# Kernel optimization log

Measured on AMD Instinct MI355X. Metric: run time of the kernel, lower is better.

## Reference

```python
import jax, jax.numpy as jnp
import numpy as np

D = 512  # common_dim

def _ln(x, g, b):
    m = jnp.mean(x, -1, keepdims=True)
    v = jnp.var(x, -1, keepdims=True)
    return g * (x - m) * jax.lax.rsqrt(v + 1e-5) + b

def _gelu(x):
    return jax.nn.gelu(x, approximate=False)  # torch nn.GELU default (erf)

def _mha(q, kv, Wi, bi, Wo, bo):
    # seq_len == 1: softmax over a single key is exactly 1 regardless of q/k,
    # so MultiheadAttention reduces to out_proj(v_proj(kv)); identical math,
    # and q/k projections receive exactly zero gradient either way.
    vp = kv @ Wi[:, 2 * D:] + bi[2 * D:]
    return vp @ Wo + bo

def setup_inputs() -> dict:
    key = jax.random.key(0)
    ks = iter(jax.random.split(key, 64))
    B, HID = 8192, 1024
    Fv, Fi, Ft = 10, 6, 15
    def rn(shape, s=0.02):
        return jax.random.normal(next(ks), shape, jnp.float32) * s
    return dict(
        verb_hidden=rn((B, HID), 1.0), verb_logits=rn((B, Fv), 1.0),
        inst_hidden=rn((B, HID), 1.0), inst_logits=rn((B, Fi), 1.0),
        target_hidden=rn((B, HID), 1.0), target_logits=rn((B, Ft), 1.0),
        # hidden_projection per task (order: verb, instrument, target)
        hp_W=rn((3, HID, D)), hp_b=jnp.zeros((3, D)), hp_g=jnp.ones((3, D)), hp_be=jnp.zeros((3, D)),
        # logit_projection per task (different in-dims)
        lp_W_verb=rn((Fv, D // 2)), lp_b_verb=jnp.zeros((D // 2,)),
        lp_W_inst=rn((Fi, D // 2)), lp_b_inst=jnp.zeros((D // 2,)),
        lp_W_target=rn((Ft, D // 2)), lp_b_target=jnp.zeros((D // 2,)),
        lp_g=jnp.ones((3, D // 2)), lp_be=jnp.zeros((3, D // 2)),
        # 4 MHA modules: [self, verb_inst, verb_target, inst_target]
        mha_in_W=rn((4, D, 3 * D)), mha_in_b=jnp.zeros((4, 3 * D)),
        mha_out_W=rn((4, D, D)), mha_out_b=jnp.zeros((4, D)),
        n1_g=jnp.ones((3, D)), n1_be=jnp.zeros((3, D)),
        n2_g=jnp.ones((3, D)), n2_be=jnp.zeros((3, D)),
        gate_W=rn((3, 2 * D, D)), gate_b=jnp.zeros((3, D)),
        fus_W1=rn((3 * D + 3 * (D // 2), D)), fus_b1=jnp.zeros((D,)),
        fus_g1=jnp.ones((D,)), fus_ge1=jnp.zeros((D,)),
        fus_W2=rn((D, D)), fus_b2=jnp.zeros((D,)),
        fus_g2=jnp.ones((D,)), fus_ge2=jnp.zeros((D,)),
    )

def reference(verb_hidden, verb_logits, inst_hidden, inst_logits, target_hidden, target_logits,
              hp_W, hp_b, hp_g, hp_be,
              lp_W_verb, lp_b_verb, lp_W_inst, lp_b_inst, lp_W_target, lp_b_target, lp_g, lp_be,
              mha_in_W, mha_in_b, mha_out_W, mha_out_b,
              n1_g, n1_be, n2_g, n2_be, gate_W, gate_b,
              fus_W1, fus_b1, fus_g1, fus_ge1, fus_W2, fus_b2, fus_g2, fus_ge2):
    # dropout is inference-mode identity
    def hproj(x, i):
        return _gelu(_ln(x @ hp_W[i] + hp_b[i], hp_g[i], hp_be[i]))
    def lproj(x, W, b, i):
        return _gelu(_ln(jax.nn.sigmoid(x) @ W + b, lp_g[i], lp_be[i]))

    verb_h, inst_h, target_h = hproj(verb_hidden, 0), hproj(inst_hidden, 1), hproj(target_hidden, 2)
    verb_l = lproj(verb_logits, lp_W_verb, lp_b_verb, 0)
    inst_l = lproj(inst_logits, lp_W_inst, lp_b_inst, 1)
    target_l = lproj(target_logits, lp_W_target, lp_b_target, 2)

    sa = lambda x: _mha(x, x, mha_in_W[0], mha_in_b[0], mha_out_W[0], mha_out_b[0])
    verb_e = _ln(verb_h + sa(verb_h), n1_g[0], n1_be[0])
    inst_e = _ln(inst_h + sa(inst_h), n1_g[1], n1_be[1])
    target_e = _ln(target_h + sa(target_h), n1_g[2], n1_be[2])

    ca = lambda i, q, kv: _mha(q, kv, mha_in_W[i], mha_in_b[i], mha_out_W[i], mha_out_b[i])
    v2i, i2v = ca(1, verb_e, inst_e), ca(1, inst_e, verb_e)
    v2t, t2v = ca(2, verb_e, target_e), ca(2, target_e, verb_e)
    i2t, t2i = ca(3, inst_e, target_e), ca(3, target_e, inst_e)

    def fuse(x, a, b, i):
        m = (a + b) * 0.5
        gate = jax.nn.sigmoid(jnp.concatenate([x, m], axis=1) @ gate_W[i] + gate_b[i])
        return _ln(x + gate * m, n2_g[i], n2_be[i])

    verb_f = fuse(verb_e, v2i, v2t, 0)
    inst_f = fuse(inst_e, i2v, i2t, 1)
    target_f = fuse(target_e, t2v, t2i, 2)

    comb = jnp.concatenate([verb_f, inst_f, target_f, verb_l, inst_l, target_l], axis=1)  # [B, 2304]
    h = _gelu(_ln(comb @ fus_W1 + fus_b1, fus_g1, fus_ge1))
    return _ln(h @ fus_W2 + fus_b2, fus_g2, fus_ge2)
```

## Files before the change

kernel.cpp:

```cpp
#include <hip/hip_runtime.h>
#include <math.h>

typedef unsigned short ushort_t;
using short8  = __attribute__((ext_vector_type(8))) short;
using floatx4 = __attribute__((ext_vector_type(4))) float;

__device__ __forceinline__ ushort_t f2bf(float f) {
  unsigned u = __builtin_bit_cast(unsigned, f);
  u = (u + 0x7fffu + ((u >> 16) & 1u)) >> 16;
  return (ushort_t)u;
}
__device__ __forceinline__ float bf2f(ushort_t u) {
  unsigned v = ((unsigned)u) << 16;
  return __builtin_bit_cast(float, v);
}

__device__ __forceinline__ void load_lds16(const ushort_t* g, ushort_t* l) {
  __builtin_amdgcn_global_load_lds(
      (const __attribute__((address_space(1))) unsigned int*)g,
      (__attribute__((address_space(3))) unsigned int*)l, 16, 0, 0);
}

struct Seg { const ushort_t* A; const ushort_t* W; int lda, ldw, K; };
struct GemmZ {
  ushort_t* Cb;
  ushort_t* CbT;
  const float* bias;
  float scale; int nseg; int mmax;
  Seg seg[6];
};
struct GemmArgs { GemmZ z[9]; };

template <int BM>
__global__ __launch_bounds__(256) void gemm_bt(GemmArgs ga) {
  const GemmZ& gz = ga.z[blockIdx.z];
  if ((int)blockIdx.x >= gz.mmax) return;
  __shared__ ushort_t As[BM * 32];
  __shared__ ushort_t Bs[128 * 32];
  const int tid = threadIdx.x;
  const int wid = tid >> 6, lane = tid & 63, quad = lane >> 4, l16 = lane & 15;
  const int bm = blockIdx.x * BM, bn = blockIdx.y * 128;
  constexpr int MI = BM / 32;
  const int wm = (wid & 1) * (BM / 2), wn = (wid >> 1) * 64;
  floatx4 acc[MI][4] = {};
  const int srow = tid >> 2, scol = (tid & 3) * 8;
  ushort_t* aL = As + tid * 8;
  ushort_t* bL = Bs + tid * 8;

  for (int s = 0; s < gz.nseg; s++) {
    const Seg sg = gz.seg[s];
    const ushort_t* aG = sg.A + (size_t)(bm + srow) * sg.lda + scol;
    const ushort_t* bG = sg.W + (size_t)(bn + srow) * sg.ldw + scol;
    const size_t astep = (size_t)64 * sg.lda;
    const size_t bstep = (size_t)64 * sg.ldw;
    for (int k0 = 0; k0 < sg.K; k0 += 32) {
      __syncthreads();
      load_lds16(aG + k0, aL);
      if (BM == 128) load_lds16(aG + k0 + astep, aL + 2048);
      load_lds16(bG + k0, bL);
      load_lds16(bG + k0 + bstep, bL + 2048);
      __syncthreads();
      short8 af[MI], bf[4];
#pragma unroll
      for (int i = 0; i < MI; i++)
        af[i] = *(const short8*)&As[(wm + 16 * i + l16) * 32 + quad * 8];
#pragma unroll
      for (int j = 0; j < 4; j++)
        bf[j] = *(const short8*)&Bs[(wn + 16 * j + l16) * 32 + quad * 8];
#pragma unroll
      for (int i = 0; i < MI; i++)
#pragma unroll
        for (int j = 0; j < 4; j++)
          acc[i][j] = __builtin_amdgcn_mfma_f32_16x16x32_bf16(af[i], bf[j], acc[i][j], 0, 0, 0);
    }
  }

#pragma unroll
  for (int i = 0; i < MI; i++) {
#pragma unroll
    for (int j = 0; j < 4; j++) {
      const int colg = bn + wn + 16 * j + l16;
      const float bb = gz.bias ? gz.bias[colg] : 0.f;
#pragma unroll
      for (int r = 0; r < 4; r++) {
        const int rowg = bm + wm + 16 * i + quad * 4 + r;
        const float v = (acc[i][j][r] + bb) * gz.scale;
        const ushort_t bo = f2bf(v);
        if (gz.Cb)  gz.Cb[(size_t)rowg * 512 + colg] = bo;
        if (gz.CbT) gz.CbT[(size_t)colg * 512 + rowg] = bo;
      }
    }
  }
}

__global__ __launch_bounds__(256) void row_ln(
    const ushort_t* __restrict__ P, const ushort_t* __restrict__ R,
    const ushort_t* __restrict__ cross,
    const float* __restrict__ gamma, const float* __restrict__ beta, int gstride,
    ushort_t* __restrict__ outb, float* __restrict__ outf, int mode, int gelu)
{
  const size_t S2 = (size_t)8192 * 512;
  const int wid = threadIdx.x >> 6, lane = threadIdx.x & 63;
  const int row = blockIdx.x * 4 + wid;
  const int t = row >> 13;
  const float* g  = gamma + t * gstride;
  const float* be = beta + t * gstride;
  const ushort_t* p = P + (size_t)row * 512;
  const ushort_t* ar = nullptr;
  if (mode == 2) ar = cross + (size_t)(2 * t) * S2 + (size_t)(row & 8191) * 512;
  float v[8], s = 0.f, ss = 0.f;
#pragma unroll
  for (int j = 0; j < 8; j++) {
    const int c = lane + j * 64;
    float x = bf2f(p[c]);
    if (mode == 2) {
      const float sg = 1.f / (1.f + expf(-x));
      x = bf2f(R[(size_t)row * 512 + c]) + sg * (bf2f(ar[c]) + bf2f(ar[S2 + c]));
    } else if (mode == 1) {
      x += bf2f(R[(size_t)row * 512 + c]);
    }
    v[j] = x; s += x; ss += x * x;
  }
#pragma unroll
  for (int off = 32; off > 0; off >>= 1) {
    s  += __shfl_xor(s,  off, 64);
    ss += __shfl_xor(ss, off, 64);
  }
  const float mean = s * (1.f / 512.f);
  const float var  = ss * (1.f / 512.f) - mean * mean;
  const float rstd = rsqrtf(var + 1e-5f);
#pragma unroll
  for (int j = 0; j < 8; j++) {
    const int c = lane + j * 64;
    float y = g[c] * ((v[j] - mean) * rstd) + be[c];
    if (gelu) y = 0.5f * y * (1.f + erff(y * 0.70710678118f));
    if (outb) outb[(size_t)row * 512 + c] = f2bf(y);
    else      outf[(size_t)row * 512 + c] = y;
  }
}

__global__ __launch_bounds__(256) void lproj3(
    const float* __restrict__ vl, const float* __restrict__ il, const float* __restrict__ tl,
    const float* __restrict__ Wv, const float* __restrict__ bv,
    const float* __restrict__ Wi, const float* __restrict__ bi,
    const float* __restrict__ Wt, const float* __restrict__ bt,
    const float* __restrict__ lp_g, const float* __restrict__ lp_be,
    ushort_t* __restrict__ out)
{
  const int set = blockIdx.y;
  const float* logits = set == 0 ? vl : set == 1 ? il : tl;
  const int F = set == 0 ? 10 : set == 1 ? 6 : 15;
  const float* W    = set == 0 ? Wv : set == 1 ? Wi : Wt;
  const float* bias = set == 0 ? bv : set == 1 ? bi : bt;
  const float* gamma = lp_g + set * 256;
  const float* beta  = lp_be + set * 256;
  ushort_t* o = out + (size_t)set * 8192 * 256;
  const int wid = threadIdx.x >> 6, lane = threadIdx.x & 63;
  const int row = blockIdx.x * 4 + wid;
  float sg[16];
  for (int f = 0; f < F; f++)
    sg[f] = 1.f / (1.f + expf(-logits[(size_t)row * F + f]));
  float v[4], s = 0.f, ss = 0.f;
#pragma unroll
  for (int j = 0; j < 4; j++) {
    const int c = lane + j * 64;
    float a = bias[c];
    for (int f = 0; f < F; f++) a += sg[f] * W[f * 256 + c];
    v[j] = a; s += a; ss += a * a;
  }
#pragma unroll
  for (int off = 32; off > 0; off >>= 1) {
    s  += __shfl_xor(s,  off, 64);
    ss += __shfl_xor(ss, off, 64);
  }
  const float mean = s * (1.f / 256.f);
  const float var  = ss * (1.f / 256.f) - mean * mean;
  const float rstd = rsqrtf(var + 1e-5f);
#pragma unroll
  for (int j = 0; j < 4; j++) {
    const int c = lane + j * 64;
    float y = gamma[c] * ((v[j] - mean) * rstd) + beta[c];
    y = 0.5f * y * (1.f + erff(y * 0.70710678118f));
    o[(size_t)row * 256 + c] = f2bf(y);
  }
}

struct PrepArgs {
  const float *vh, *ih, *th;
  const float *mha_in_W, *mha_out_W, *mha_in_b, *mha_out_b;
  const float *hp_W, *gate_W, *fus_W1, *fus_W2;
  ushort_t *xbf, *Wvbf, *hpWt, *gateWt, *fusW1t, *fusW2t, *WoT;
  float *cb;
};

__global__ __launch_bounds__(256) void prep(PrepArgs pa) {
  __shared__ float tsh[32][33];
  const int b = blockIdx.x, tid = threadIdx.x;
  if (b < 24576) {
    const int mat = b >> 13, blk = b & 8191;
    const float* src = mat == 0 ? pa.vh : mat == 1 ? pa.ih : pa.th;
    const size_t i = (size_t)blk * 256 + tid;
    const float4 f = ((const float4*)src)[i];
    ushort4 o; o.x = f2bf(f.x); o.y = f2bf(f.y); o.z = f2bf(f.z); o.w = f2bf(f.w);
    ((ushort4*)(pa.xbf + (size_t)mat * 8192 * 1024))[i] = o;
    return;
  }
  if (b < 28672) {
    const int u = b - 24576, z = u >> 10, blk = u & 1023;
    const int idx = blk * 256 + tid, r = idx >> 9, c = idx & 511;
    pa.Wvbf[(size_t)z * 262144 + idx] =
        f2bf(pa.mha_in_W[(size_t)z * 786432 + (size_t)r * 1536 + 1024 + c]);
    return;
  }
  if (b >= 34176) {
    const int u2 = b - 34176, z = u2 >> 1, part = u2 & 1;
    const int n = part * 256 + tid;
    const float* bv = pa.mha_in_b + z * 1536 + 1024;
    const float* Wo = pa.mha_out_W + (size_t)z * 262144;
    float a = pa.mha_out_b[z * 512 + n];
    for (int k = 0; k < 512; k++) a += bv[k] * Wo[(size_t)k * 512 + n];
    pa.cb[z * 512 + n] = a;
    return;
  }
  const float* tin; ushort_t* tout; int K, N, u; size_t izs, ozs;
  if (b < 30208)      { u = b - 28672; tin = pa.hp_W;      tout = pa.hpWt;   K = 1024; N = 512; izs = 524288; ozs = 524288; }
  else if (b < 31744) { u = b - 30208; tin = pa.gate_W;    tout = pa.gateWt; K = 1024; N = 512; izs = 524288; ozs = 524288; }
  else if (b < 32896) { u = b - 31744; tin = pa.fus_W1;    tout = pa.fusW1t; K = 2304; N = 512; izs = 0;      ozs = 0; }
  else if (b < 33152) { u = b - 32896; tin = pa.fus_W2;    tout = pa.fusW2t; K = 512;  N = 512; izs = 0;      ozs = 0; }
  else                { u = b - 33152; tin = pa.mha_out_W; tout = pa.WoT;    K = 512;  N = 512; izs = 262144; ozs = 262144; }
  const int nbx = N / 32, perz = nbx * (K / 32);
  const int z = u / perz, rem = u % perz, bx = rem % nbx, by = rem / nbx;
  tin += (size_t)z * izs; tout += (size_t)z * ozs;
  const int n0 = bx * 32, k0 = by * 32;
  const int tx = tid & 31, ty = tid >> 5;
#pragma unroll
  for (int r = 0; r < 32; r += 8)
    tsh[ty + r][tx] = tin[(size_t)(k0 + ty + r) * N + n0 + tx];
  __syncthreads();
#pragma unroll
  for (int r = 0; r < 32; r += 8)
    tout[(size_t)(n0 + ty + r) * K + k0 + tx] = f2bf(tsh[tx][ty + r]);
}

__global__ __launch_bounds__(256) void bias2_k(
    const float* __restrict__ cb, const float* __restrict__ gate_W,
    const float* __restrict__ gate_b, float* __restrict__ out)
{
  const int t = blockIdx.z;
  const int m1[3] = {1, 1, 2}, m2[3] = {2, 3, 3};
  const float* c1 = cb + m1[t] * 512;
  const float* c2 = cb + m2[t] * 512;
  const float* W = gate_W + (size_t)t * 524288 + (size_t)512 * 512;
  const int n = blockIdx.x * 256 + threadIdx.x;
  float a = gate_b[t * 512 + n];
  for (int k = 0; k < 512; k++) a += 0.5f * (c1[k] + c2[k]) * W[(size_t)k * 512 + n];
  out[t * 512 + n] = a;
}

extern "C" void kernel_launch(void* const* d_in, const int* in_sizes, int n_in,
                              void* d_out, int out_size, void* d_ws, size_t ws_size,
                              hipStream_t stream)
{
  const float* verb_hidden   = (const float*)d_in[0];
  const float* verb_logits   = (const float*)d_in[1];
  const float* inst_hidden   = (const float*)d_in[2];
  const float* inst_logits   = (const float*)d_in[3];
  const float* target_hidden = (const float*)d_in[4];
  const float* target_logits = (const float*)d_in[5];
  const float* hp_W  = (const float*)d_in[6];
  const float* hp_b  = (const float*)d_in[7];
  const float* hp_g  = (const float*)d_in[8];
  const float* hp_be = (const float*)d_in[9];
  const float* lp_W_verb   = (const float*)d_in[10];
  const float* lp_b_verb   = (const float*)d_in[11];
  const float* lp_W_inst   = (const float*)d_in[12];
  const float* lp_b_inst   = (const float*)d_in[13];
  const float* lp_W_target = (const float*)d_in[14];
  const float* lp_b_target = (const float*)d_in[15];
  const float* lp_g  = (const float*)d_in[16];
  const float* lp_be = (const float*)d_in[17];
  const float* mha_in_W  = (const float*)d_in[18];
  const float* mha_in_b  = (const float*)d_in[19];
  const float* mha_out_W = (const float*)d_in[20];
  const float* mha_out_b = (const float*)d_in[21];
  const float* n1_g  = (const float*)d_in[22];
  const float* n1_be = (const float*)d_in[23];
  const float* n2_g  = (const float*)d_in[24];
  const float* n2_be = (const float*)d_in[25];
  const float* gate_W = (const float*)d_in[26];
  const float* gate_b = (const float*)d_in[27];
  const float* fus_W1 = (const float*)d_in[28];
  const float* fus_b1 = (const float*)d_in[29];
  const float* fus_g1 = (const float*)d_in[30];
  const float* fus_ge1= (const float*)d_in[31];
  const float* fus_W2 = (const float*)d_in[32];
  const float* fus_b2 = (const float*)d_in[33];
  const float* fus_g2 = (const float*)d_in[34];
  const float* fus_ge2= (const float*)d_in[35];

  char* w = (char*)d_ws;
  const size_t S2 = (size_t)8192 * 512;
  const size_t MB = 1024 * 1024;
  ushort_t* xbf     = (ushort_t*)(w);
  ushort_t* crossbf = (ushort_t*)(w);
  ushort_t* gbf     = (ushort_t*)(w);
  ushort_t* Pbig    = (ushort_t*)(w + 48 * MB);
  ushort_t* hbf     = (ushort_t*)(w + 72 * MB);
  ushort_t* fbf     = (ushort_t*)(w + 72 * MB);
  ushort_t* ebf     = (ushort_t*)(w + 96 * MB);
  ushort_t* lbf     = (ushort_t*)(w + 120 * MB);
  char* wp = w + 132 * MB;
  ushort_t* hpWt    = (ushort_t*)(wp);
  ushort_t* gateWt  = (ushort_t*)(wp + 3145728);
  ushort_t* fusW1t  = (ushort_t*)(wp + 6291456);
  ushort_t* fusW2t  = (ushort_t*)(wp + 8650752);
  ushort_t* WoT     = (ushort_t*)(wp + 9175040);
  ushort_t* Wvbf    = (ushort_t*)(wp + 11272192);
  ushort_t* CWt     = (ushort_t*)(wp + 13369344);
  ushort_t* CWplain = (ushort_t*)(wp + 15466496);
  ushort_t* Gt      = (ushort_t*)(wp + 17563648);
  float*    cb      = (float*)(wp + 20709376);
  float*    bias2   = (float*)(wp + 20717568);

  dim3 blk(256);
  const int mods[3][2] = {{1, 2}, {1, 3}, {2, 3}};
  const int srcs[3][2] = {{1, 2}, {0, 2}, {0, 1}};

  {
    PrepArgs pa;
    pa.vh = verb_hidden; pa.ih = inst_hidden; pa.th = target_hidden;
    pa.mha_in_W = mha_in_W; pa.mha_out_W = mha_out_W;
    pa.mha_in_b = mha_in_b; pa.mha_out_b = mha_out_b;
    pa.hp_W = hp_W; pa.gate_W = gate_W; pa.fus_W1 = fus_W1; pa.fus_W2 = fus_W2;
    pa.xbf = xbf; pa.Wvbf = Wvbf; pa.hpWt = hpWt; pa.gateWt = gateWt;
    pa.fusW1t = fusW1t; pa.fusW2t = fusW2t; pa.WoT = WoT; pa.cb = cb;
    prep<<<34184, blk, 0, stream>>>(pa);
  }

  {
    GemmArgs ga{};
    for (int z = 0; z < 4; z++) {
      GemmZ& g = ga.z[z];
      g.Cb = CWplain + (size_t)z * 262144; g.CbT = CWt + (size_t)z * 262144;
      g.scale = 1.f; g.nseg = 1; g.mmax = 4;
      g.seg[0] = {Wvbf + (size_t)z * 262144, WoT + (size_t)z * 262144, 512, 512, 512};
    }
    gemm_bt<128><<<dim3(4, 4, 4), blk, 0, stream>>>(ga);
  }

  bias2_k<<<dim3(2, 1, 3), blk, 0, stream>>>(cb, gate_W, gate_b, bias2);

  {
    GemmArgs ga{};
    for (int z = 0; z < 3; z++) {
      GemmZ& g = ga.z[z];
      g.Cb = Pbig + (size_t)z * S2; g.bias = hp_b + z * 512;
      g.scale = 1.f; g.nseg = 1; g.mmax = 64;
      g.seg[0] = {xbf + (size_t)z * 8192 * 1024, hpWt + (size_t)z * 524288, 1024, 1024, 1024};
    }
    for (int idx = 0; idx < 6; idx++) {
      const int t = idx >> 1, u = idx & 1, m = mods[t][u];
      GemmZ& g = ga.z[3 + idx];
      g.Cb = Gt + (size_t)idx * 262144; g.scale = 0.5f; g.nseg = 1; g.mmax = 4;
      g.seg[0] = {gateWt + (size_t)t * 524288 + 512, CWplain + (size_t)m * 262144, 1024, 512, 512};
    }
    gemm_bt<128><<<dim3(64, 4, 9), blk, 0, stream>>>(ga);
  }

  lproj3<<<dim3(2048, 3), blk, 0, stream>>>(verb_logits, inst_logits, target_logits,
      lp_W_verb, lp_b_verb, lp_W_inst, lp_b_inst, lp_W_target, lp_b_target,
      lp_g, lp_be, lbf);

  row_ln<<<6144, blk, 0, stream>>>(Pbig, nullptr, nullptr, hp_g, hp_be, 512,
                                   hbf, nullptr, 0, 1);

  {
    GemmArgs ga{};
    GemmZ& g = ga.z[0];
    g.Cb = Pbig; g.bias = cb; g.scale = 1.f; g.nseg = 1; g.mmax = 192;
    g.seg[0] = {hbf, CWt, 512, 512, 512};
    gemm_bt<128><<<dim3(192, 4, 1), blk, 0, stream>>>(ga);
  }
  row_ln<<<6144, blk, 0, stream>>>(Pbig, hbf, nullptr, n1_g, n1_be, 512,
                                   ebf, nullptr, 1, 0);

  {
    GemmArgs ga{};
    for (int t = 0; t < 3; t++)
      for (int u = 0; u < 2; u++) {
        GemmZ& g = ga.z[2 * t + u];
        g.Cb = crossbf + (size_t)(2 * t + u) * S2;
        g.bias = cb + mods[t][u] * 512; g.scale = 0.5f; g.nseg = 1; g.mmax = 64;
        g.seg[0] = {ebf + (size_t)srcs[t][u] * S2, CWt + (size_t)mods[t][u] * 262144, 512, 512, 512};
      }
    for (int t = 0; t < 3; t++) {
      GemmZ& g = ga.z[6 + t];
      g.Cb = Pbig + (size_t)t * S2; g.bias = bias2 + t * 512;
      g.scale = 1.f; g.nseg = 3; g.mmax = 64;
      g.seg[0] = {ebf + (size_t)t * S2,           gateWt + (size_t)t * 524288, 512, 1024, 512};
      g.seg[1] = {ebf + (size_t)srcs[t][0] * S2,  Gt + (size_t)(2 * t) * 262144,     512, 512, 512};
      g.seg[2] = {ebf + (size_t)srcs[t][1] * S2,  Gt + (size_t)(2 * t + 1) * 262144, 512, 512, 512};
    }
    gemm_bt<128><<<dim3(64, 4, 9), blk, 0, stream>>>(ga);
  }

  row_ln<<<6144, blk, 0, stream>>>(Pbig, ebf, crossbf, n2_g, n2_be, 512,
                                   fbf, nullptr, 2, 0);

  {
    GemmArgs ga{};
    GemmZ& g = ga.z[0];
    g.Cb = Pbig; g.bias = fus_b1; g.scale = 1.f; g.nseg = 6; g.mmax = 128;
    g.seg[0] = {fbf,                          fusW1t,        512, 2304, 512};
    g.seg[1] = {fbf + S2,                     fusW1t + 512,  512, 2304, 512};
    g.seg[2] = {fbf + 2 * S2,                 fusW1t + 1024, 512, 2304, 512};
    g.seg[3] = {lbf,                          fusW1t + 1536, 256, 2304, 256};
    g.seg[4] = {lbf + (size_t)8192 * 256,     fusW1t + 1792, 256, 2304, 256};
    g.seg[5] = {lbf + (size_t)2 * 8192 * 256, fusW1t + 2048, 256, 2304, 256};
    gemm_bt<64><<<dim3(128, 4, 1), blk, 0, stream>>>(ga);
  }
  row_ln<<<2048, blk, 0, stream>>>(Pbig, nullptr, nullptr, fus_g1, fus_ge1, 0,
                                   gbf, nullptr, 0, 1);
  {
    GemmArgs ga{};
    GemmZ& g = ga.z[0];
    g.Cb = Pbig; g.bias = fus_b2; g.scale = 1.f; g.nseg = 1; g.mmax = 128;
    g.seg[0] = {gbf, fusW2t, 512, 512, 512};
    gemm_bt<64><<<dim3(128, 4, 1), blk, 0, stream>>>(ga);
  }
  row_ln<<<2048, blk, 0, stream>>>(Pbig, nullptr, nullptr, fus_g2, fus_ge2, 0,
                                   nullptr, (float*)d_out, 0, 0);
}
```

Measured before the change: 669.8 us.

## Fuse LayerNorm epilogues into full-row GEMM and convert fp32 inputs in-kernel

Replaces the tiled GEMM plus separate row LayerNorm kernels with one GEMM kernel that computes a full 512-wide output row block (32 rows × 512 cols, 512 threads). Residual add, sigmoid gating, LayerNorm and GELU are done in the epilogue through a cross-wave LDS reduction. This removes the bf16 intermediate round trips through global memory and the separate row_ln launches. The hidden-projection GEMM now reads the fp32 inputs directly and converts them to bf16 while staging, so the prep conversion pass is dropped. In exchange, M tiles are smaller (32 rows), each block holds the whole 512×32 B tile, and the fp32 A path uses narrow non-vectorized loads, which could hurt GEMM efficiency.

```diff
diff --git a/kernel.cpp b/kernel.cpp
--- a/kernel.cpp
+++ b/kernel.cpp
@@ -14,129 +14,159 @@
   unsigned v = ((unsigned)u) << 16;
   return __builtin_bit_cast(float, v);
 }
-
 __device__ __forceinline__ void load_lds16(const ushort_t* g, ushort_t* l) {
   __builtin_amdgcn_global_load_lds(
       (const __attribute__((address_space(1))) unsigned int*)g,
       (__attribute__((address_space(3))) unsigned int*)l, 16, 0, 0);
 }
 
-struct Seg { const ushort_t* A; const ushort_t* W; int lda, ldw, K; };
+struct Seg { const void* A; const ushort_t* W; int lda, ldw, K, a_f32; };
 struct GemmZ {
-  ushort_t* Cb;
-  ushort_t* CbT;
+  ushort_t* Cb; ushort_t* CbT; float* Cf;
   const float* bias;
-  float scale; int nseg; int mmax;
+  const ushort_t* R; const ushort_t* crA; const ushort_t* crB;
+  const float* gamma; const float* beta;
+  float scale; int gstride;
+  int nseg, mmax, mode, gelu;
   Seg seg[6];
 };
 struct GemmArgs { GemmZ z[9]; };
 
-template <int BM>
-__global__ __launch_bounds__(256) void gemm_bt(GemmArgs ga) {
+__global__ __launch_bounds__(512) void gemm_fln(GemmArgs ga) {
   const GemmZ& gz = ga.z[blockIdx.z];
   if ((int)blockIdx.x >= gz.mmax) return;
-  __shared__ ushort_t As[BM * 32];
-  __shared__ ushort_t Bs[128 * 32];
+  __shared__ ushort_t Bs[512 * 32];
+  __shared__ ushort_t As[32 * 32];
+  __shared__ float redS[32][8], redSS[32][8];
+  __shared__ float lnM[32], lnR[32];
   const int tid = threadIdx.x;
   const int wid = tid >> 6, lane = tid & 63, quad = lane >> 4, l16 = lane & 15;
-  const int bm = blockIdx.x * BM, bn = blockIdx.y * 128;
-  constexpr int MI = BM / 32;
-  const int wm = (wid & 1) * (BM / 2), wn = (wid >> 1) * 64;
-  floatx4 acc[MI][4] = {};
-  const int srow = tid >> 2, scol = (tid & 3) * 8;
-  ushort_t* aL = As + tid * 8;
-  ushort_t* bL = Bs + tid * 8;
+  const int bm = blockIdx.x * 32;
+  const int wn = wid * 64;
+  floatx4 acc[2][4] = {};
 
   for (int s = 0; s < gz.nseg; s++) {
     const Seg sg = gz.seg[s];
-    const ushort_t* aG = sg.A + (size_t)(bm + srow) * sg.lda + scol;
-    const ushort_t* bG = sg.W + (size_t)(bn + srow) * sg.ldw + scol;
-    const size_t astep = (size_t)64 * sg.lda;
-    const size_t bstep = (size_t)64 * sg.ldw;
     for (int k0 = 0; k0 < sg.K; k0 += 32) {
       __syncthreads();
-      load_lds16(aG + k0, aL);
-      if (BM == 128) load_lds16(aG + k0 + astep, aL + 2048);
-      load_lds16(bG + k0, bL);
-      load_lds16(bG + k0 + bstep, bL + 2048);
+#pragma unroll
+      for (int q = 0; q < 4; q++)
+        load_lds16(sg.W + (size_t)(q * 128 + (tid >> 2)) * sg.ldw + k0 + (tid & 3) * 8,
+                   Bs + q * 4096 + tid * 8);
+      if (sg.a_f32) {
+        const float* Af = (const float*)sg.A;
+        const int ar = tid >> 4, ak = (tid & 15) * 2;
+        const float* src = Af + (size_t)(bm + ar) * sg.lda + k0 + ak;
+        ushort2 h; h.x = f2bf(src[0]); h.y = f2bf(src[1]);
+        *(ushort2*)&As[ar * 32 + ak] = h;
+      } else if (tid < 128) {
+        load_lds16((const ushort_t*)sg.A + (size_t)(bm + (tid >> 2)) * sg.lda + k0 + (tid & 3) * 8,
+                   As + tid * 8);
+      }
       __syncthreads();
-      short8 af[MI], bf[4];
-#pragma unroll
-      for (int i = 0; i < MI; i++)
-        af[i] = *(const short8*)&As[(wm + 16 * i + l16) * 32 + quad * 8];
+      short8 af[2], bf[4];
+#pragma unroll
+      for (int i = 0; i < 2; i++)
+        af[i] = *(const short8*)&As[(16 * i + l16) * 32 + quad * 8];
 #pragma unroll
       for (int j = 0; j < 4; j++)
         bf[j] = *(const short8*)&Bs[(wn + 16 * j + l16) * 32 + quad * 8];
 #pragma unroll
-      for (int i = 0; i < MI; i++)
+      for (int i = 0; i < 2; i++)
 #pragma unroll
         for (int j = 0; j < 4; j++)
           acc[i][j] = __builtin_amdgcn_mfma_f32_16x16x32_bf16(af[i], bf[j], acc[i][j], 0, 0, 0);
     }
   }
 
-#pragma unroll
-  for (int i = 0; i < MI; i++) {
+  if (gz.mode < 0) {
+#pragma unroll
+    for (int i = 0; i < 2; i++)
+#pragma unroll
+      for (int j = 0; j < 4; j++) {
+        const int col = wn + 16 * j + l16;
+        const float bb = gz.bias ? gz.bias[col] : 0.f;
+#pragma unroll
+        for (int r = 0; r < 4; r++) {
+          const int rowg = bm + 16 * i + quad * 4 + r;
+          const ushort_t bo = f2bf((acc[i][j][r] + bb) * gz.scale);
+          if (gz.Cb)  gz.Cb[(size_t)rowg * 512 + col] = bo;
+          if (gz.CbT) gz.CbT[(size_t)col * 512 + rowg] = bo;
+        }
+      }
+    return;
+  }
+
+  const int task = gz.gstride ? (bm >> 13) : 0;
+  const float* gam = gz.gamma + task * gz.gstride;
+  const float* bet = gz.beta  + task * gz.gstride;
+
+  float s_p[2][4] = {}, ss_p[2][4] = {};
+#pragma unroll
+  for (int i = 0; i < 2; i++)
 #pragma unroll
     for (int j = 0; j < 4; j++) {
-      const int colg = bn + wn + 16 * j + l16;
-      const float bb = gz.bias ? gz.bias[colg] : 0.f;
+      const int col = wn + 16 * j + l16;
+      const float bb = gz.bias ? gz.bias[col] : 0.f;
 #pragma unroll
       for (int r = 0; r < 4; r++) {
-        const int rowg = bm + wm + 16 * i + quad * 4 + r;
-        const float v = (acc[i][j][r] + bb) * gz.scale;
-        const ushort_t bo = f2bf(v);
-        if (gz.Cb)  gz.Cb[(size_t)rowg * 512 + colg] = bo;
-        if (gz.CbT) gz.CbT[(size_t)colg * 512 + rowg] = bo;
-      }
-    }
-  }
-}
-
-__global__ __launch_bounds__(256) void row_ln(
-    const ushort_t* __restrict__ P, const ushort_t* __restrict__ R,
-    const ushort_t* __restrict__ cross,
-    const float* __restrict__ gamma, const float* __restrict__ beta, int gstride,
-    ushort_t* __restrict__ outb, float* __restrict__ outf, int mode, int gelu)
-{
-  const size_t S2 = (size_t)8192 * 512;
-  const int wid = threadIdx.x >> 6, lane = threadIdx.x & 63;
-  const int row = blockIdx.x * 4 + wid;
-  const int t = row >> 13;
-  const float* g  = gamma + t * gstride;
-  const float* be = beta + t * gstride;
-  const ushort_t* p = P + (size_t)row * 512;
-  const ushort_t* ar = nullptr;
-  if (mode == 2) ar = cross + (size_t)(2 * t) * S2 + (size_t)(row & 8191) * 512;
-  float v[8], s = 0.f, ss = 0.f;
-#pragma unroll
-  for (int j = 0; j < 8; j++) {
-    const int c = lane + j * 64;
-    float x = bf2f(p[c]);
-    if (mode == 2) {
-      const float sg = 1.f / (1.f + expf(-x));
-      x = bf2f(R[(size_t)row * 512 + c]) + sg * (bf2f(ar[c]) + bf2f(ar[S2 + c]));
-    } else if (mode == 1) {
-      x += bf2f(R[(size_t)row * 512 + c]);
-    }
-    v[j] = x; s += x; ss += x * x;
-  }
-#pragma unroll
-  for (int off = 32; off > 0; off >>= 1) {
-    s  += __shfl_xor(s,  off, 64);
-    ss += __shfl_xor(ss, off, 64);
-  }
-  const float mean = s * (1.f / 512.f);
-  const float var  = ss * (1.f / 512.f) - mean * mean;
-  const float rstd = rsqrtf(var + 1e-5f);
-#pragma unroll
-  for (int j = 0; j < 8; j++) {
-    const int c = lane + j * 64;
-    float y = g[c] * ((v[j] - mean) * rstd) + be[c];
-    if (gelu) y = 0.5f * y * (1.f + erff(y * 0.70710678118f));
-    if (outb) outb[(size_t)row * 512 + c] = f2bf(y);
-    else      outf[(size_t)row * 512 + c] = y;
-  }
+        const int rowg = bm + 16 * i + quad * 4 + r;
+        float x = acc[i][j][r] + bb;
+        if (gz.mode == 1) {
+          x += bf2f(gz.R[(size_t)rowg * 512 + col]);
+        } else if (gz.mode == 2) {
+          const float sg = 1.f / (1.f + expf(-x));
+          x = bf2f(gz.R[(size_t)rowg * 512 + col]) +
+              sg * (bf2f(gz.crA[(size_t)rowg * 512 + col]) +
+                    bf2f(gz.crB[(size_t)rowg * 512 + col]));
+        }
+        acc[i][j][r] = x;
+        s_p[i][r] += x; ss_p[i][r] += x * x;
+      }
+    }
+#pragma unroll
+  for (int m = 1; m <= 8; m <<= 1)
+#pragma unroll
+    for (int i = 0; i < 2; i++)
+#pragma unroll
+      for (int r = 0; r < 4; r++) {
+        s_p[i][r]  += __shfl_xor(s_p[i][r],  m, 64);
+        ss_p[i][r] += __shfl_xor(ss_p[i][r], m, 64);
+      }
+  if (l16 == 0) {
+#pragma unroll
+    for (int i = 0; i < 2; i++)
+#pragma unroll
+      for (int r = 0; r < 4; r++) {
+        redS[16 * i + quad * 4 + r][wid]  = s_p[i][r];
+        redSS[16 * i + quad * 4 + r][wid] = ss_p[i][r];
+      }
+  }
+  __syncthreads();
+  if (tid < 32) {
+    float s = 0.f, ss = 0.f;
+#pragma unroll
+    for (int wv = 0; wv < 8; wv++) { s += redS[tid][wv]; ss += redSS[tid][wv]; }
+    const float mean = s * (1.f / 512.f);
+    const float var  = ss * (1.f / 512.f) - mean * mean;
+    lnM[tid] = mean; lnR[tid] = rsqrtf(var + 1e-5f);
+  }
+  __syncthreads();
+#pragma unroll
+  for (int i = 0; i < 2; i++)
+#pragma unroll
+    for (int j = 0; j < 4; j++) {
+      const int col = wn + 16 * j + l16;
+#pragma unroll
+      for (int r = 0; r < 4; r++) {
+        const int rl = 16 * i + quad * 4 + r;
+        const int rowg = bm + rl;
+        float y = gam[col] * ((acc[i][j][r] - lnM[rl]) * lnR[rl]) + bet[col];
+        if (gz.gelu) y = 0.5f * y * (1.f + erff(y * 0.70710678118f));
+        if (gz.Cf) gz.Cf[(size_t)rowg * 512 + col] = y;
+        else       gz.Cb[(size_t)rowg * 512 + col] = f2bf(y);
+      }
+    }
 }
 
 __global__ __launch_bounds__(256) void lproj3(
@@ -186,34 +216,24 @@
 }
 
 struct PrepArgs {
-  const float *vh, *ih, *th;
   const float *mha_in_W, *mha_out_W, *mha_in_b, *mha_out_b;
   const float *hp_W, *gate_W, *fus_W1, *fus_W2;
-  ushort_t *xbf, *Wvbf, *hpWt, *gateWt, *fusW1t, *fusW2t, *WoT;
+  ushort_t *Wvbf, *hpWt, *gateWt, *fusW1t, *fusW2t, *WoT;
   float *cb;
 };
 
 __global__ __launch_bounds__(256) void prep(PrepArgs pa) {
   __shared__ float tsh[32][33];
   const int b = blockIdx.x, tid = threadIdx.x;
-  if (b < 24576) {
-    const int mat = b >> 13, blk = b & 8191;
-    const float* src = mat == 0 ? pa.vh : mat == 1 ? pa.ih : pa.th;
-    const size_t i = (size_t)blk * 256 + tid;
-    const float4 f = ((const float4*)src)[i];
-    ushort4 o; o.x = f2bf(f.x); o.y = f2bf(f.y); o.z = f2bf(f.z); o.w = f2bf(f.w);
-    ((ushort4*)(pa.xbf + (size_t)mat * 8192 * 1024))[i] = o;
-    return;
-  }
-  if (b < 28672) {
-    const int u = b - 24576, z = u >> 10, blk = u & 1023;
+  if (b < 4096) {
+    const int z = b >> 10, blk = b & 1023;
     const int idx = blk * 256 + tid, r = idx >> 9, c = idx & 511;
     pa.Wvbf[(size_t)z * 262144 + idx] =
         f2bf(pa.mha_in_W[(size_t)z * 786432 + (size_t)r * 1536 + 1024 + c]);
     return;
   }
-  if (b >= 34176) {
-    const int u2 = b - 34176, z = u2 >> 1, part = u2 & 1;
+  if (b >= 9600) {
+    const int u2 = b - 9600, z = u2 >> 1, part = u2 & 1;
     const int n = part * 256 + tid;
     const float* bv = pa.mha_in_b + z * 1536 + 1024;
     const float* Wo = pa.mha_out_W + (size_t)z * 262144;
@@ -223,11 +243,11 @@
     return;
   }
   const float* tin; ushort_t* tout; int K, N, u; size_t izs, ozs;
-  if (b < 30208)      { u = b - 28672; tin = pa.hp_W;      tout = pa.hpWt;   K = 1024; N = 512; izs = 524288; ozs = 524288; }
-  else if (b < 31744) { u = b - 30208; tin = pa.gate_W;    tout = pa.gateWt; K = 1024; N = 512; izs = 524288; ozs = 524288; }
-  else if (b < 32896) { u = b - 31744; tin = pa.fus_W1;    tout = pa.fusW1t; K = 2304; N = 512; izs = 0;      ozs = 0; }
-  else if (b < 33152) { u = b - 32896; tin = pa.fus_W2;    tout = pa.fusW2t; K = 512;  N = 512; izs = 0;      ozs = 0; }
-  else                { u = b - 33152; tin = pa.mha_out_W; tout = pa.WoT;    K = 512;  N = 512; izs = 262144; ozs = 262144; }
+  if (b < 5632)      { u = b - 4096; tin = pa.hp_W;      tout = pa.hpWt;   K = 1024; N = 512; izs = 524288; ozs = 524288; }
+  else if (b < 7168) { u = b - 5632; tin = pa.gate_W;    tout = pa.gateWt; K = 1024; N = 512; izs = 524288; ozs = 524288; }
+  else if (b < 8320) { u = b - 7168; tin = pa.fus_W1;    tout = pa.fusW1t; K = 2304; N = 512; izs = 0;      ozs = 0; }
+  else if (b < 8576) { u = b - 8320; tin = pa.fus_W2;    tout = pa.fusW2t; K = 512;  N = 512; izs = 0;      ozs = 0; }
+  else               { u = b - 8576; tin = pa.mha_out_W; tout = pa.WoT;    K = 512;  N = 512; izs = 262144; ozs = 262144; }
   const int nbx = N / 32, perz = nbx * (K / 32);
   const int z = u / perz, rem = u % perz, bx = rem % nbx, by = rem / nbx;
   tin += (size_t)z * izs; tout += (size_t)z * ozs;
@@ -301,15 +321,13 @@
   char* w = (char*)d_ws;
   const size_t S2 = (size_t)8192 * 512;
   const size_t MB = 1024 * 1024;
-  ushort_t* xbf     = (ushort_t*)(w);
   ushort_t* crossbf = (ushort_t*)(w);
   ushort_t* gbf     = (ushort_t*)(w);
-  ushort_t* Pbig    = (ushort_t*)(w + 48 * MB);
-  ushort_t* hbf     = (ushort_t*)(w + 72 * MB);
-  ushort_t* fbf     = (ushort_t*)(w + 72 * MB);
-  ushort_t* ebf     = (ushort_t*)(w + 96 * MB);
-  ushort_t* lbf     = (ushort_t*)(w + 120 * MB);
-  char* wp = w + 132 * MB;
+  ushort_t* hbf     = (ushort_t*)(w + 48 * MB);
+  ushort_t* fbf     = (ushort_t*)(w + 48 * MB);
+  ushort_t* ebf     = (ushort_t*)(w + 72 * MB);
+  ushort_t* lbf     = (ushort_t*)(w + 96 * MB);
+  char* wp = w + 108 * MB;
   ushort_t* hpWt    = (ushort_t*)(wp);
   ushort_t* gateWt  = (ushort_t*)(wp + 3145728);
   ushort_t* fusW1t  = (ushort_t*)(wp + 6291456);
@@ -322,19 +340,18 @@
   float*    cb      = (float*)(wp + 20709376);
   float*    bias2   = (float*)(wp + 20717568);
 
-  dim3 blk(256);
+  dim3 blk256(256), blk512(512);
   const int mods[3][2] = {{1, 2}, {1, 3}, {2, 3}};
   const int srcs[3][2] = {{1, 2}, {0, 2}, {0, 1}};
 
   {
     PrepArgs pa;
-    pa.vh = verb_hidden; pa.ih = inst_hidden; pa.th = target_hidden;
     pa.mha_in_W = mha_in_W; pa.mha_out_W = mha_out_W;
     pa.mha_in_b = mha_in_b; pa.mha_out_b = mha_out_b;
     pa.hp_W = hp_W; pa.gate_W = gate_W; pa.fus_W1 = fus_W1; pa.fus_W2 = fus_W2;
-    pa.xbf = xbf; pa.Wvbf = Wvbf; pa.hpWt = hpWt; pa.gateWt = gateWt;
+    pa.Wvbf = Wvbf; pa.hpWt = hpWt; pa.gateWt = gateWt;
     pa.fusW1t = fusW1t; pa.fusW2t = fusW2t; pa.WoT = WoT; pa.cb = cb;
-    prep<<<34184, blk, 0, stream>>>(pa);
+    prep<<<9608, blk256, 0, stream>>>(pa);
   }
 
   {
@@ -342,47 +359,46 @@
     for (int z = 0; z < 4; z++) {
       GemmZ& g = ga.z[z];
       g.Cb = CWplain + (size_t)z * 262144; g.CbT = CWt + (size_t)z * 262144;
-      g.scale = 1.f; g.nseg = 1; g.mmax = 4;
-      g.seg[0] = {Wvbf + (size_t)z * 262144, WoT + (size_t)z * 262144, 512, 512, 512};
-    }
-    gemm_bt<128><<<dim3(4, 4, 4), blk, 0, stream>>>(ga);
-  }
-
-  bias2_k<<<dim3(2, 1, 3), blk, 0, stream>>>(cb, gate_W, gate_b, bias2);
-
-  {
-    GemmArgs ga{};
+      g.scale = 1.f; g.nseg = 1; g.mmax = 16; g.mode = -1;
+      g.seg[0] = {Wvbf + (size_t)z * 262144, WoT + (size_t)z * 262144, 512, 512, 512, 0};
+    }
+    gemm_fln<<<dim3(16, 1, 4), blk512, 0, stream>>>(ga);
+  }
+
+  bias2_k<<<dim3(2, 1, 3), blk256, 0, stream>>>(cb, gate_W, gate_b, bias2);
+
+  {
+    GemmArgs ga{};
+    const float* xs[3] = {verb_hidden, inst_hidden, target_hidden};
     for (int z = 0; z < 3; z++) {
       GemmZ& g = ga.z[z];
-      g.Cb = Pbig + (size_t)z * S2; g.bias = hp_b + z * 512;
-      g.scale = 1.f; g.nseg = 1; g.mmax = 64;
-      g.seg[0] = {xbf + (size_t)z * 8192 * 1024, hpWt + (size_t)z * 524288, 1024, 1024, 1024};
+      g.Cb = hbf + (size_t)z * S2; g.bias = hp_b + z * 512;
+      g.gamma = hp_g + z * 512; g.beta = hp_be + z * 512;
+      g.scale = 1.f; g.nseg = 1; g.mmax = 256; g.mode = 0; g.gelu = 1;
+      g.seg[0] = {xs[z], hpWt + (size_t)z * 524288, 1024, 1024, 1024, 1};
     }
     for (int idx = 0; idx < 6; idx++) {
       const int t = idx >> 1, u = idx & 1, m = mods[t][u];
       GemmZ& g = ga.z[3 + idx];
-      g.Cb = Gt + (size_t)idx * 262144; g.scale = 0.5f; g.nseg = 1; g.mmax = 4;
-      g.seg[0] = {gateWt + (size_t)t * 524288 + 512, CWplain + (size_t)m * 262144, 1024, 512, 512};
-    }
-    gemm_bt<128><<<dim3(64, 4, 9), blk, 0, stream>>>(ga);
-  }
-
-  lproj3<<<dim3(2048, 3), blk, 0, stream>>>(verb_logits, inst_logits, target_logits,
+      g.Cb = Gt + (size_t)idx * 262144; g.scale = 0.5f; g.nseg = 1; g.mmax = 16; g.mode = -1;
+      g.seg[0] = {gateWt + (size_t)t * 524288 + 512, CWplain + (size_t)m * 262144, 1024, 512, 512, 0};
+    }
+    gemm_fln<<<dim3(256, 1, 9), blk512, 0, stream>>>(ga);
+  }
+
+  lproj3<<<dim3(2048, 3), blk256, 0, stream>>>(verb_logits, inst_logits, target_logits,
       lp_W_verb, lp_b_verb, lp_W_inst, lp_b_inst, lp_W_target, lp_b_target,
       lp_g, lp_be, lbf);
 
-  row_ln<<<6144, blk, 0, stream>>>(Pbig, nullptr, nullptr, hp_g, hp_be, 512,
-                                   hbf, nullptr, 0, 1);
-
   {
     GemmArgs ga{};
     GemmZ& g = ga.z[0];
-    g.Cb = Pbig; g.bias = cb; g.scale = 1.f; g.nseg = 1; g.mmax = 192;
-    g.seg[0] = {hbf, CWt, 512, 512, 512};
-    gemm_bt<128><<<dim3(192, 4, 1), blk, 0, stream>>>(ga);
-  }
-  row_ln<<<6144, blk, 0, stream>>>(Pbig, hbf, nullptr, n1_g, n1_be, 512,
-                                   ebf, nullptr, 1, 0);
+    g.Cb = ebf; g.bias = cb; g.R = hbf;
+    g.gamma = n1_g; g.beta = n1_be; g.gstride = 512;
+    g.scale = 1.f; g.nseg = 1; g.mmax = 768; g.mode = 1;
+    g.seg[0] = {hbf, CWt, 512, 512, 512, 0};
+    gemm_fln<<<dim3(768, 1, 1), blk512, 0, stream>>>(ga);
+  }
 
   {
     GemmArgs ga{};
@@ -390,44 +406,52 @@
       for (int u = 0; u < 2; u++) {
         GemmZ& g = ga.z[2 * t + u];
         g.Cb = crossbf + (size_t)(2 * t + u) * S2;
-        g.bias = cb + mods[t][u] * 512; g.scale = 0.5f; g.nseg = 1; g.mmax = 64;
-        g.seg[0] = {ebf + (size_t)srcs[t][u] * S2, CWt + (size_t)mods[t][u] * 262144, 512, 512, 512};
-      }
+        g.bias = cb + mods[t][u] * 512; g.scale = 0.5f;
+        g.nseg = 1; g.mmax = 256; g.mode = -1;
+        g.seg[0] = {ebf + (size_t)srcs[t][u] * S2, CWt + (size_t)mods[t][u] * 262144, 512, 512, 512, 0};
+      }
+    gemm_fln<<<dim3(256, 1, 6), blk512, 0, stream>>>(ga);
+  }
+
+  {
+    GemmArgs ga{};
     for (int t = 0; t < 3; t++) {
-      GemmZ& g = ga.z[6 + t];
-      g.Cb = Pbig + (size_t)t * S2; g.bias = bias2 + t * 512;
-      g.scale = 1.f; g.nseg = 3; g.mmax = 64;
-      g.seg[0] = {ebf + (size_t)t * S2,           gateWt + (size_t)t * 524288, 512, 1024, 512};
-      g.seg[1] = {ebf + (size_t)srcs[t][0] * S2,  Gt + (size_t)(2 * t) * 262144,     512, 512, 512};
-      g.seg[2] = {ebf + (size_t)srcs[t][1] * S2,  Gt + (size_t)(2 * t + 1) * 262144, 512, 512, 512};
-    }
-    gemm_bt<128><<<dim3(64, 4, 9), blk, 0, stream>>>(ga);
-  }
-
-  row_ln<<<6144, blk, 0, stream>>>(Pbig, ebf, crossbf, n2_g, n2_be, 512,
-                                   fbf, nullptr, 2, 0);
+      GemmZ& g = ga.z[t];
+      g.Cb = fbf + (size_t)t * S2; g.bias = bias2 + t * 512;
+      g.R = ebf + (size_t)t * S2;
+      g.crA = crossbf + (size_t)(2 * t) * S2;
+      g.crB = crossbf + (size_t)(2 * t + 1) * S2;
+      g.gamma = n2_g + t * 512; g.beta = n2_be + t * 512;
+      g.scale = 1.f; g.nseg = 3; g.mmax = 256; g.mode = 2;
+      g.seg[0] = {ebf + (size_t)t * S2,           gateWt + (size_t)t * 524288,       512, 1024, 512, 0};
+      g.seg[1] = {ebf + (size_t)srcs[t][0] * S2,  Gt + (size_t)(2 * t) * 262144,     512, 512,  512, 0};
+      g.seg[2] = {ebf + (size_t)srcs[t][1] * S2,  Gt + (size_t)(2 * t + 1) * 262144, 512, 512,  512, 0};
+    }
+    gemm_fln<<<dim3(256, 1, 3), blk512, 0, stream>>>(ga);
+  }
 
   {
     GemmArgs ga{};
     GemmZ& g = ga.z[0];
-    g.Cb = Pbig; g.bias = fus_b1; g.scale = 1.f; g.nseg = 6; g.mmax = 128;
-    g.seg[0] = {fbf,                          fusW1t,        512, 2304, 512};
-    g.seg[1] = {fbf + S2,                     fusW1t + 512,  512, 2304, 512};
-    g.seg[2] = {fbf + 2 * S2,                 fusW1t + 1024, 512, 2304, 512};
-    g.seg[3] = {lbf,                          fusW1t + 1536, 256, 2304, 256};
-    g.seg[4] = {lbf + (size_t)8192 * 256,     fusW1t + 1792, 256, 2304, 256};
-    g.seg[5] = {lbf + (size_t)2 * 8192 * 256, fusW1t + 2048, 256, 2304, 256};
-    gemm_bt<64><<<dim3(128, 4, 1), blk, 0, stream>>>(ga);
-  }
-  row_ln<<<2048, blk, 0, stream>>>(Pbig, nullptr, nullptr, fus_g1, fus_ge1, 0,
-                                   gbf, nullptr, 0, 1);
+    g.Cb = gbf; g.bias = fus_b1;
+    g.gamma = fus_g1; g.beta = fus_ge1;
+    g.scale = 1.f; g.nseg = 6; g.mmax = 256; g.mode = 0; g.gelu = 1;
+    g.seg[0] = {fbf,                          fusW1t,        512, 2304, 512, 0};
+    g.seg[1] = {fbf + S2,                     fusW1t + 512,  512, 2304, 512, 0};
+    g.seg[2] = {fbf + 2 * S2,                 fusW1t + 1024, 512, 2304, 512, 0};
+    g.seg[3] = {lbf,                          fusW1t + 1536, 256, 2304, 256, 0};
+    g.seg[4] = {lbf + (size_t)8192 * 256,     fusW1t + 1792, 256, 2304, 256, 0};
+    g.seg[5] = {lbf + (size_t)2 * 8192 * 256, fusW1t + 2048, 256, 2304, 256, 0};
+    gemm_fln<<<dim3(256, 1, 1), blk512, 0, stream>>>(ga);
+  }
+
   {
     GemmArgs ga{};
     GemmZ& g = ga.z[0];
-    g.Cb = Pbig; g.bias = fus_b2; g.scale = 1.f; g.nseg = 1; g.mmax = 128;
-    g.seg[0] = {gbf, fusW2t, 512, 512, 512};
-    gemm_bt<64><<<dim3(128, 4, 1), blk, 0, stream>>>(ga);
-  }
-  row_ln<<<2048, blk, 0, stream>>>(Pbig, nullptr, nullptr, fus_g2, fus_ge2, 0,
-                                   nullptr, (float*)d_out, 0, 0);
-}
+    g.Cf = (float*)d_out; g.bias = fus_b2;
+    g.gamma = fus_g2; g.beta = fus_ge2;
+    g.scale = 1.f; g.nseg = 1; g.mmax = 256; g.mode = 0;
+    g.seg[0] = {gbf, fusW2t, 512, 512, 512, 0};
+    gemm_fln<<<dim3(256, 1, 1), blk512, 0, stream>>>(ga);
+  }
+}
```

Result: slower. 828.0 us (+23.6%).

## Split-K the hidden and fusion GEMMs and shrink the self-attn GEMM tile

Applied to the files above, without the earlier changes.

The hidden-projection GEMM (K=1024) is split into two K=512 halves written to separate buffers, and the fusion GEMM is split into a hidden-part and a logits-part, also into separate buffers. The following row_ln sums the partials (residual mode), so each launch has more blocks and shorter per-block K loops. The self-attention GEMM switches from 128-row to 64-row tiles, doubling its grid. This fills more CUs on the GPU, at the cost of extra bf16 partial-buffer traffic and a little precision loss from rounding the partials.

```diff
diff --git a/kernel.cpp b/kernel.cpp
--- a/kernel.cpp
+++ b/kernel.cpp
@@ -14,7 +14,6 @@
   unsigned v = ((unsigned)u) << 16;
   return __builtin_bit_cast(float, v);
 }
-
 __device__ __forceinline__ void load_lds16(const ushort_t* g, ushort_t* l) {
   __builtin_amdgcn_global_load_lds(
       (const __attribute__((address_space(1))) unsigned int*)g,
@@ -29,7 +28,7 @@
   float scale; int nseg; int mmax;
   Seg seg[6];
 };
-struct GemmArgs { GemmZ z[9]; };
+struct GemmArgs { GemmZ z[12]; };
 
 template <int BM>
 __global__ __launch_bounds__(256) void gemm_bt(GemmArgs ga) {
@@ -321,6 +320,7 @@
   ushort_t* Gt      = (ushort_t*)(wp + 17563648);
   float*    cb      = (float*)(wp + 20709376);
   float*    bias2   = (float*)(wp + 20717568);
+  ushort_t* P2      = (ushort_t*)(w + 156 * MB);
 
   dim3 blk(256);
   const int mods[3][2] = {{1, 2}, {1, 3}, {2, 3}};
@@ -352,34 +352,37 @@
 
   {
     GemmArgs ga{};
-    for (int z = 0; z < 3; z++) {
-      GemmZ& g = ga.z[z];
-      g.Cb = Pbig + (size_t)z * S2; g.bias = hp_b + z * 512;
-      g.scale = 1.f; g.nseg = 1; g.mmax = 64;
-      g.seg[0] = {xbf + (size_t)z * 8192 * 1024, hpWt + (size_t)z * 524288, 1024, 1024, 1024};
-    }
+    for (int t = 0; t < 3; t++)
+      for (int h = 0; h < 2; h++) {
+        GemmZ& g = ga.z[2 * t + h];
+        g.Cb = (h == 0 ? Pbig : P2) + (size_t)t * S2;
+        g.bias = (h == 0) ? hp_b + t * 512 : nullptr;
+        g.scale = 1.f; g.nseg = 1; g.mmax = 64;
+        g.seg[0] = {xbf + (size_t)t * 8192 * 1024 + h * 512,
+                    hpWt + (size_t)t * 524288 + h * 512, 1024, 1024, 512};
+      }
     for (int idx = 0; idx < 6; idx++) {
       const int t = idx >> 1, u = idx & 1, m = mods[t][u];
-      GemmZ& g = ga.z[3 + idx];
+      GemmZ& g = ga.z[6 + idx];
       g.Cb = Gt + (size_t)idx * 262144; g.scale = 0.5f; g.nseg = 1; g.mmax = 4;
       g.seg[0] = {gateWt + (size_t)t * 524288 + 512, CWplain + (size_t)m * 262144, 1024, 512, 512};
     }
-    gemm_bt<128><<<dim3(64, 4, 9), blk, 0, stream>>>(ga);
+    gemm_bt<128><<<dim3(64, 4, 12), blk, 0, stream>>>(ga);
   }
 
   lproj3<<<dim3(2048, 3), blk, 0, stream>>>(verb_logits, inst_logits, target_logits,
       lp_W_verb, lp_b_verb, lp_W_inst, lp_b_inst, lp_W_target, lp_b_target,
       lp_g, lp_be, lbf);
 
-  row_ln<<<6144, blk, 0, stream>>>(Pbig, nullptr, nullptr, hp_g, hp_be, 512,
-                                   hbf, nullptr, 0, 1);
+  row_ln<<<6144, blk, 0, stream>>>(Pbig, P2, nullptr, hp_g, hp_be, 512,
+                                   hbf, nullptr, 1, 1);
 
   {
     GemmArgs ga{};
     GemmZ& g = ga.z[0];
-    g.Cb = Pbig; g.bias = cb; g.scale = 1.f; g.nseg = 1; g.mmax = 192;
+    g.Cb = Pbig; g.bias = cb; g.scale = 1.f; g.nseg = 1; g.mmax = 384;
     g.seg[0] = {hbf, CWt, 512, 512, 512};
-    gemm_bt<128><<<dim3(192, 4, 1), blk, 0, stream>>>(ga);
+    gemm_bt<64><<<dim3(384, 4, 1), blk, 0, stream>>>(ga);
   }
   row_ln<<<6144, blk, 0, stream>>>(Pbig, hbf, nullptr, n1_g, n1_be, 512,
                                    ebf, nullptr, 1, 0);
@@ -409,18 +412,20 @@
 
   {
     GemmArgs ga{};
-    GemmZ& g = ga.z[0];
-    g.Cb = Pbig; g.bias = fus_b1; g.scale = 1.f; g.nseg = 6; g.mmax = 128;
-    g.seg[0] = {fbf,                          fusW1t,        512, 2304, 512};
-    g.seg[1] = {fbf + S2,                     fusW1t + 512,  512, 2304, 512};
-    g.seg[2] = {fbf + 2 * S2,                 fusW1t + 1024, 512, 2304, 512};
-    g.seg[3] = {lbf,                          fusW1t + 1536, 256, 2304, 256};
-    g.seg[4] = {lbf + (size_t)8192 * 256,     fusW1t + 1792, 256, 2304, 256};
-    g.seg[5] = {lbf + (size_t)2 * 8192 * 256, fusW1t + 2048, 256, 2304, 256};
-    gemm_bt<64><<<dim3(128, 4, 1), blk, 0, stream>>>(ga);
-  }
-  row_ln<<<2048, blk, 0, stream>>>(Pbig, nullptr, nullptr, fus_g1, fus_ge1, 0,
-                                   gbf, nullptr, 0, 1);
+    GemmZ& g0 = ga.z[0];
+    g0.Cb = Pbig; g0.bias = fus_b1; g0.scale = 1.f; g0.nseg = 3; g0.mmax = 128;
+    g0.seg[0] = {fbf,          fusW1t,        512, 2304, 512};
+    g0.seg[1] = {fbf + S2,     fusW1t + 512,  512, 2304, 512};
+    g0.seg[2] = {fbf + 2 * S2, fusW1t + 1024, 512, 2304, 512};
+    GemmZ& g1 = ga.z[1];
+    g1.Cb = P2; g1.scale = 1.f; g1.nseg = 3; g1.mmax = 128;
+    g1.seg[0] = {lbf,                          fusW1t + 1536, 256, 2304, 256};
+    g1.seg[1] = {lbf + (size_t)8192 * 256,     fusW1t + 1792, 256, 2304, 256};
+    g1.seg[2] = {lbf + (size_t)2 * 8192 * 256, fusW1t + 2048, 256, 2304, 256};
+    gemm_bt<64><<<dim3(128, 4, 2), blk, 0, stream>>>(ga);
+  }
+  row_ln<<<2048, blk, 0, stream>>>(Pbig, P2, nullptr, fus_g1, fus_ge1, 0,
+                                   gbf, nullptr, 1, 1);
   {
     GemmArgs ga{};
     GemmZ& g = ga.z[0];
```

Result: slower. 686.4 us (+2.5%).
